# Performance work log

Hardware: AMD Instinct MI355X
Metric: run time of the kernel (lower is better)

Reference implementation:

```python
import jax, jax.numpy as jnp
import numpy as np

B, C, C2, E = 4, 1024, 1024, 1024
D = 1024          # context_size (d_q = d_kv)
NH = 16           # module's n_heads arg -> actual head_dim after the quirky view
G = D // NH       # effective number of head groups = 64


def setup_inputs() -> dict:
    key = jax.random.key(0)
    ks = jax.random.split(key, 6)
    s = 0.02
    return {
        "x1": jax.random.normal(ks[0], (B, C, E), dtype=jnp.float32),
        "x2": jax.random.normal(ks[1], (B, C2, E), dtype=jnp.float32),
        "W_q": jax.random.normal(ks[2], (E, D), dtype=jnp.float32) * s,
        "W_k": jax.random.normal(ks[3], (E, D), dtype=jnp.float32) * s,
        "W_v": jax.random.normal(ks[4], (E, D), dtype=jnp.float32) * s,
        "W_o": jax.random.normal(ks[5], (D, D), dtype=jnp.float32) * s,
    }


def _split_heads(t):
    # (B, S, D) -> view (B, S, G, NH) -> transpose(1,2) -> (B, G, S, NH)
    b, s, _ = t.shape
    return jnp.transpose(t.reshape(b, s, G, NH), (0, 2, 1, 3))


def reference(x1, x2, W_q, W_k, W_v, W_o):
    Q = _split_heads(x1 @ W_q)   # (B, G, C, NH)
    K = _split_heads(x2 @ W_k)   # (B, G, C2, NH)
    V = _split_heads(x2 @ W_v)   # (B, G, C2, NH)
    scale = 1.0 / jnp.sqrt(jnp.asarray(NH, dtype=Q.dtype))
    scores = jnp.einsum("bgqh,bgkh->bgqk", Q, K) * scale  # (B, G, C, C2)
    w = jax.nn.softmax(scores, axis=-1)
    out = jnp.einsum("bgqk,bgkh->bgqh", w, V)             # (B, G, C, NH)
    out = jnp.transpose(out, (0, 2, 1, 3)).reshape(B, C, D)
    return out @ W_o  # dropout p=0 -> identity
```

## Files before the change

kernel.cpp:

```cpp
#include <hip/hip_runtime.h>


typedef _Float16 f16x8 __attribute__((ext_vector_type(8)));
typedef _Float16 f16x4 __attribute__((ext_vector_type(4)));
typedef _Float16 f16x2 __attribute__((ext_vector_type(2)));
typedef float    f32x4 __attribute__((ext_vector_type(4)));
typedef float    f32x16 __attribute__((ext_vector_type(16)));

#define GLOAD_LDS16(gp, lp)                                              \
    __builtin_amdgcn_global_load_lds(                                    \
        (const __attribute__((address_space(1))) void*)(gp),             \
        (__attribute__((address_space(3))) void*)(lp), 16, 0, 0)

static __device__ __forceinline__ f16x8 pack8f(const float* p) {
    f16x2 a = __builtin_bit_cast(f16x2, __builtin_amdgcn_cvt_pkrtz(p[0], p[1]));
    f16x2 b = __builtin_bit_cast(f16x2, __builtin_amdgcn_cvt_pkrtz(p[2], p[3]));
    f16x2 c = __builtin_bit_cast(f16x2, __builtin_amdgcn_cvt_pkrtz(p[4], p[5]));
    f16x2 d = __builtin_bit_cast(f16x2, __builtin_amdgcn_cvt_pkrtz(p[6], p[7]));
    f16x8 r;
    r[0] = a[0]; r[1] = a[1]; r[2] = b[0]; r[3] = b[1];
    r[4] = c[0]; r[5] = c[1]; r[6] = d[0]; r[7] = d[1];
    return r;
}

__global__ __launch_bounds__(256) void prep_kernel(
        const float* __restrict__ x1, const float* __restrict__ x2,
        const float* __restrict__ W0, const float* __restrict__ W1,
        const float* __restrict__ W2, const float* __restrict__ W3,
        _Float16* __restrict__ y1, _Float16* __restrict__ y2,
        _Float16* __restrict__ T0, _Float16* __restrict__ T1,
        _Float16* __restrict__ T2, _Float16* __restrict__ T3) {
    int bx = blockIdx.x, tid = threadIdx.x;
    if (bx < 8192) {
        int i = bx * 256 + tid;
        const float* x = (i < 1048576) ? x1 : x2;
        _Float16* y = (i < 1048576) ? y1 : y2;
        int j = i & 1048575;
        float4 v = ((const float4*)x)[j];
        f16x4 h = { (_Float16)v.x, (_Float16)v.y, (_Float16)v.z, (_Float16)v.w };
        ((f16x4*)y)[j] = h;
    } else {
        int z = (bx - 8192) >> 10;
        const float* W = (z == 0) ? W0 : (z == 1) ? W1 : (z == 2) ? W2 : W3;
        _Float16* WT = (z == 0) ? T0 : (z == 1) ? T1 : (z == 2) ? T2 : T3;
        int t = (bx - 8192) & 1023;
        int c0 = (t & 31) * 32, r0 = (t >> 5) * 32;
        __shared__ float tile[32][33];
        int tx = tid & 31, ty = tid >> 5;
#pragma unroll
        for (int i = 0; i < 32; i += 8)
            tile[ty + i][tx] = W[(r0 + ty + i) * 1024 + (c0 + tx)];
        __syncthreads();
#pragma unroll
        for (int i = 0; i < 32; i += 8)
            WT[(c0 + ty + i) * 1024 + (r0 + tx)] = (_Float16)tile[tx][ty + i];
    }
}

template <int MT, bool OUTF32>
static __device__ __forceinline__ void gemm_body(const _Float16* __restrict__ Atile,
                                                 const _Float16* __restrict__ BTtile,
                                                 void* __restrict__ Ctile,
                                                 _Float16* As, _Float16* Bs) {
    constexpr int AF = MT / 32;
    const int tid = threadIdx.x, lane = tid & 63, wave = tid >> 6;
    const int wm = wave >> 1, wn = wave & 1;
    const int col = lane & 15, quad = lane >> 4;

    f32x4 acc[AF][4];
#pragma unroll
    for (int i = 0; i < AF; i++)
#pragma unroll
        for (int j = 0; j < 4; j++) acc[i][j] = (f32x4){0.f, 0.f, 0.f, 0.f};

    const int srow = wave * 8 + (lane >> 3);
    const int sch = (lane & 7) * 8;
    const _Float16* Ag = Atile + (size_t)srow * 1024 + sch;
    const _Float16* Bg = BTtile + (size_t)srow * 1024 + sch;
    _Float16* Asl = As + wave * 512;
    _Float16* Bsl = Bs + wave * 512;

    for (int kt = 0; kt < 16; kt++) {
        __syncthreads();
#pragma unroll
        for (int c = 0; c < AF; c++)
            GLOAD_LDS16(Ag + (size_t)(c * 32) * 1024 + kt * 64, Asl + c * 2048);
#pragma unroll
        for (int c = 0; c < 4; c++)
            GLOAD_LDS16(Bg + (size_t)(c * 32) * 1024 + kt * 64, Bsl + c * 2048);
        __syncthreads();
#pragma unroll
        for (int ki = 0; ki < 2; ki++) {
            f16x8 af[AF], bf[4];
#pragma unroll
            for (int i = 0; i < AF; i++)
                af[i] = *(const f16x8*)(As + (wm * (MT / 2) + i * 16 + col) * 64 + ki * 32 + quad * 8);
#pragma unroll
            for (int j = 0; j < 4; j++)
                bf[j] = *(const f16x8*)(Bs + (wn * 64 + j * 16 + col) * 64 + ki * 32 + quad * 8);
#pragma unroll
            for (int i = 0; i < AF; i++)
#pragma unroll
                for (int j = 0; j < 4; j++)
                    acc[i][j] = __builtin_amdgcn_mfma_f32_16x16x32_f16(af[i], bf[j], acc[i][j], 0, 0, 0);
        }
    }

#pragma unroll
    for (int i = 0; i < AF; i++)
#pragma unroll
        for (int ii = 0; ii < 4; ii++) {
            int row = wm * (MT / 2) + i * 16 + quad * 4 + ii;
#pragma unroll
            for (int j = 0; j < 4; j++) {
                int cc = wn * 64 + j * 16 + col;
                if (OUTF32) ((float*)Ctile)[(size_t)row * 1024 + cc] = acc[i][j][ii];
                else ((_Float16*)Ctile)[(size_t)row * 1024 + cc] = (_Float16)acc[i][j][ii];
            }
        }
}

__global__ __launch_bounds__(256, 3) void gemm_qkv_kernel(
        const _Float16* __restrict__ x1h, const _Float16* __restrict__ x2h,
        const _Float16* __restrict__ WqT, const _Float16* __restrict__ WkvT,
        _Float16* __restrict__ Qh, _Float16* __restrict__ Kh, _Float16* __restrict__ Vh) {
    __shared__ _Float16 As[128 * 64], Bs[128 * 64];
    int gx = blockIdx.x;
    const _Float16 *A, *BT;
    _Float16* C;
    int m0, n0;
    if (gx < 256) {
        m0 = (gx >> 3) * 128; n0 = (gx & 7) * 128;
        A = x1h; BT = WqT + (size_t)n0 * 1024; C = Qh + n0;
    } else {
        int idx = gx - 256;
        m0 = (idx >> 4) * 128;
        int nb = idx & 15;
        n0 = nb * 128;
        A = x2h; BT = WkvT + (size_t)n0 * 1024;
        C = (nb < 8) ? (Kh + n0) : (Vh + (n0 - 1024));
    }
    gemm_body<128, false>(A + (size_t)m0 * 1024, BT, (void*)(C + (size_t)m0 * 1024), As, Bs);
}

__global__ __launch_bounds__(256, 4) void gemm_wo_kernel(const _Float16* __restrict__ Ah,
                                                         const _Float16* __restrict__ WoT,
                                                         float* __restrict__ out) {
    __shared__ _Float16 As[64 * 64], Bs[128 * 64];
    int gx = blockIdx.x;
    int m0 = (gx >> 3) * 64, n0 = (gx & 7) * 128;
    gemm_body<64, true>(Ah + (size_t)m0 * 1024, WoT + (size_t)n0 * 1024,
                        (void*)(out + (size_t)m0 * 1024 + n0), As, Bs);
}

__global__ __launch_bounds__(256, 8) void attn_kernel(const _Float16* __restrict__ Qh,
                                                      const _Float16* __restrict__ Kh,
                                                      const _Float16* __restrict__ Vh,
                                                      _Float16* __restrict__ Ah) {
    int pair = blockIdx.y;
    int b = pair >> 6, g = pair & 63;
    __shared__ _Float16 KA[2048];
    __shared__ _Float16 VA[2048];
    __shared__ _Float16 ones[8];

    const _Float16* Kg = Kh + (size_t)(b * 1024) * 1024 + g * 16;
    const _Float16* Vg = Vh + (size_t)(b * 1024) * 1024 + g * 16;
    int tid = threadIdx.x;
    if (tid < 8) ones[tid] = (_Float16)1.f;

    int lane = tid & 63, wave = tid >> 6;
    int n = lane & 31, h5 = lane >> 5;
    int q0 = blockIdx.x * 128 + wave * 32;

    f16x8 qf;
    {
        f16x8 t = *(const f16x8*)(Qh + (size_t)(b * 1024 + q0 + n) * 1024 + g * 16 + h5 * 8);
#pragma unroll
        for (int j = 0; j < 8; j++) qf[j] = (_Float16)((float)t[j] * 0.360673760f);
    }

    f32x16 acc = {0.f, 0.f, 0.f, 0.f, 0.f, 0.f, 0.f, 0.f,
                  0.f, 0.f, 0.f, 0.f, 0.f, 0.f, 0.f, 0.f};
    const f32x16 zero16 = acc;
    const _Float16* vbase = (n < 16) ? (VA + (n + 16 * h5) * 8) : ones;
    const int vstep = (n < 16) ? 256 : 0;

    const int krow = tid >> 1, kpart = tid & 1;
    const int kpm = (krow & 19) | ((krow & 4) << 1) | ((krow & 8) >> 1);
    const int kdst = (((krow >> 5) * 64) + kpm + 32 * kpart) * 8;
    const int vk0 = (tid >> 1) * 2 & 127, vpart = tid & 1;
    const int vbase_w = (vk0 >> 4) * 256 + ((vk0 >> 3) & 1) * 128 + vpart * 64 + (vk0 & 7);

    for (int c = 0; c < 8; c++) {
        if (c) __syncthreads();
        *(uint4*)(KA + kdst) =
            *(const uint4*)(Kg + (size_t)(c * 128 + krow) * 1024 + kpart * 8);
        if (tid < 128) {
            f16x8 v0 = *(const f16x8*)(Vg + (size_t)(c * 128 + vk0) * 1024 + vpart * 8);
            f16x8 v1 = *(const f16x8*)(Vg + (size_t)(c * 128 + vk0 + 1) * 1024 + vpart * 8);
#pragma unroll
            for (int j = 0; j < 8; j++) {
                f16x2 pr; pr[0] = v0[j]; pr[1] = v1[j];
                *(f16x2*)(VA + vbase_w + j * 8) = pr;
            }
        }
        __syncthreads();

#pragma unroll
        for (int t = 0; t < 4; t++) {
            f16x8 ak = *(const f16x8*)(KA + (t * 64 + lane) * 8);
            f32x16 s = __builtin_amdgcn_mfma_f32_32x32x16_f16(ak, qf, zero16, 0, 0, 0);
            float p[16];
#pragma unroll
            for (int i = 0; i < 16; i++) p[i] = __builtin_amdgcn_exp2f(s[i]);
            f16x8 pb0 = pack8f(p);
            f16x8 pb1 = pack8f(p + 8);
            f16x8 av0 = *(const f16x8*)(vbase + (2 * t) * vstep);
            f16x8 av1 = *(const f16x8*)(vbase + (2 * t + 1) * vstep);
            acc = __builtin_amdgcn_mfma_f32_32x32x16_f16(av0, pb0, acc, 0, 0, 0);
            acc = __builtin_amdgcn_mfma_f32_32x32x16_f16(av1, pb1, acc, 0, 0, 0);
        }
    }

    float rl = 1.0f / acc[8];
    f16x4 o0, o1;
#pragma unroll
    for (int i = 0; i < 4; i++) o0[i] = (_Float16)(acc[i] * rl);
#pragma unroll
    for (int i = 0; i < 4; i++) o1[i] = (_Float16)(acc[4 + i] * rl);
    _Float16* ob = Ah + (size_t)(b * 1024 + q0 + n) * 1024 + g * 16 + h5 * 4;
    *(f16x4*)(ob) = o0;
    *(f16x4*)(ob + 8) = o1;
}

extern "C" void kernel_launch(void* const* d_in, const int* in_sizes, int n_in,
                              void* d_out, int out_size, void* d_ws, size_t ws_size,
                              hipStream_t stream) {
    const float* x1 = (const float*)d_in[0];
    const float* x2 = (const float*)d_in[1];
    const float* Wq = (const float*)d_in[2];
    const float* Wk = (const float*)d_in[3];
    const float* Wv = (const float*)d_in[4];
    const float* Wo = (const float*)d_in[5];

    char* ws = (char*)d_ws;
    const size_t MB = 1u << 20;
    if (ws_size < 56 * MB) return;

    _Float16* x1h = (_Float16*)(ws + 0 * MB);
    _Float16* x2h = (_Float16*)(ws + 8 * MB);
    _Float16* WqT = (_Float16*)(ws + 16 * MB);
    _Float16* WkT = (_Float16*)(ws + 18 * MB);
    _Float16* WvT = (_Float16*)(ws + 20 * MB);
    _Float16* WoT = (_Float16*)(ws + 22 * MB);
    _Float16* Qh  = (_Float16*)(ws + 24 * MB);
    _Float16* Kh  = (_Float16*)(ws + 32 * MB);
    _Float16* Vh  = (_Float16*)(ws + 40 * MB);
    _Float16* Ah  = (_Float16*)(ws + 48 * MB);

    prep_kernel<<<12288, 256, 0, stream>>>(x1, x2, Wq, Wk, Wv, Wo,
                                           x1h, x2h, WqT, WkT, WvT, WoT);

    gemm_qkv_kernel<<<768, 256, 0, stream>>>(x1h, x2h, WqT, WkT, Qh, Kh, Vh);

    attn_kernel<<<dim3(8, 256), 256, 0, stream>>>(Qh, Kh, Vh, Ah);

    gemm_wo_kernel<<<512, 256, 0, stream>>>(Ah, WoT, (float*)d_out);
}
```

Before: 196.0 us.

## Prefetch next K/V chunk into registers, swizzle V LDS layout, reorder attention grid

The attention kernel now loads the next 128-key K/V chunk into registers while the current chunk is being computed, so global memory latency overlaps with MFMA and exp work. The V tile in LDS gets an XOR swizzle on both the write and read paths to reduce bank conflicts. Wave priority is raised around the compute section, and the grid axes are swapped so consecutive blocks cover different (batch, group) pairs rather than different query tiles. This costs extra registers for the prefetch buffers and precomputed offsets, which may lower occupancy.

```diff
diff --git a/kernel.cpp b/kernel.cpp
--- a/kernel.cpp
+++ b/kernel.cpp
@@ -157,7 +157,7 @@
                                                       const _Float16* __restrict__ Kh,
                                                       const _Float16* __restrict__ Vh,
                                                       _Float16* __restrict__ Ah) {
-    int pair = blockIdx.y;
+    int pair = blockIdx.x;
     int b = pair >> 6, g = pair & 63;
     __shared__ _Float16 KA[2048];
     __shared__ _Float16 VA[2048];
@@ -170,7 +170,7 @@
 
     int lane = tid & 63, wave = tid >> 6;
     int n = lane & 31, h5 = lane >> 5;
-    int q0 = blockIdx.x * 128 + wave * 32;
+    int q0 = blockIdx.y * 128 + wave * 32;
 
     f16x8 qf;
     {
@@ -182,30 +182,49 @@
     f32x16 acc = {0.f, 0.f, 0.f, 0.f, 0.f, 0.f, 0.f, 0.f,
                   0.f, 0.f, 0.f, 0.f, 0.f, 0.f, 0.f, 0.f};
     const f32x16 zero16 = acc;
-    const _Float16* vbase = (n < 16) ? (VA + (n + 16 * h5) * 8) : ones;
-    const int vstep = (n < 16) ? 256 : 0;
 
     const int krow = tid >> 1, kpart = tid & 1;
     const int kpm = (krow & 19) | ((krow & 4) << 1) | ((krow & 8) >> 1);
     const int kdst = (((krow >> 5) * 64) + kpm + 32 * kpart) * 8;
     const int vk0 = (tid >> 1) * 2 & 127, vpart = tid & 1;
-    const int vbase_w = (vk0 >> 4) * 256 + ((vk0 >> 3) & 1) * 128 + vpart * 64 + (vk0 & 7);
+    const int vbw2 = (((vk0 >> 4) * 256 + ((vk0 >> 3) & 1) * 128 + vpart * 64 + (vk0 & 7)))
+                   ^ (((vk0 >> 3) & 7) << 3);
+
+    int vaoff[8];
+#pragma unroll
+    for (int s = 0; s < 8; s++) {
+        int nsw = (n & 8) | ((n & 7) ^ (((s & 3) << 1) | h5));
+        vaoff[s] = (n < 16) ? ((s >> 2) * 1024 + (s & 3) * 256 + h5 * 128 + nsw * 8) : 0;
+    }
+    const _Float16* vrb = (n < 16) ? VA : ones;
+
+    uint4 kreg;
+    f16x8 v0, v1;
+    kreg = *(const uint4*)(Kg + (size_t)krow * 1024 + kpart * 8);
+    if (tid < 128) {
+        v0 = *(const f16x8*)(Vg + (size_t)vk0 * 1024 + vpart * 8);
+        v1 = *(const f16x8*)(Vg + (size_t)(vk0 + 1) * 1024 + vpart * 8);
+    }
 
     for (int c = 0; c < 8; c++) {
-        if (c) __syncthreads();
-        *(uint4*)(KA + kdst) =
-            *(const uint4*)(Kg + (size_t)(c * 128 + krow) * 1024 + kpart * 8);
+        __syncthreads();
+        *(uint4*)(KA + kdst) = kreg;
         if (tid < 128) {
-            f16x8 v0 = *(const f16x8*)(Vg + (size_t)(c * 128 + vk0) * 1024 + vpart * 8);
-            f16x8 v1 = *(const f16x8*)(Vg + (size_t)(c * 128 + vk0 + 1) * 1024 + vpart * 8);
 #pragma unroll
             for (int j = 0; j < 8; j++) {
                 f16x2 pr; pr[0] = v0[j]; pr[1] = v1[j];
-                *(f16x2*)(VA + vbase_w + j * 8) = pr;
+                *(f16x2*)(VA + (vbw2 ^ (j * 8))) = pr;
             }
         }
         __syncthreads();
-
+        if (c < 7) {
+            kreg = *(const uint4*)(Kg + (size_t)((c + 1) * 128 + krow) * 1024 + kpart * 8);
+            if (tid < 128) {
+                v0 = *(const f16x8*)(Vg + (size_t)((c + 1) * 128 + vk0) * 1024 + vpart * 8);
+                v1 = *(const f16x8*)(Vg + (size_t)((c + 1) * 128 + vk0 + 1) * 1024 + vpart * 8);
+            }
+        }
+        __builtin_amdgcn_s_setprio(1);
 #pragma unroll
         for (int t = 0; t < 4; t++) {
             f16x8 ak = *(const f16x8*)(KA + (t * 64 + lane) * 8);
@@ -215,11 +234,12 @@
             for (int i = 0; i < 16; i++) p[i] = __builtin_amdgcn_exp2f(s[i]);
             f16x8 pb0 = pack8f(p);
             f16x8 pb1 = pack8f(p + 8);
-            f16x8 av0 = *(const f16x8*)(vbase + (2 * t) * vstep);
-            f16x8 av1 = *(const f16x8*)(vbase + (2 * t + 1) * vstep);
+            f16x8 av0 = *(const f16x8*)(vrb + vaoff[2 * t]);
+            f16x8 av1 = *(const f16x8*)(vrb + vaoff[2 * t + 1]);
             acc = __builtin_amdgcn_mfma_f32_32x32x16_f16(av0, pb0, acc, 0, 0, 0);
             acc = __builtin_amdgcn_mfma_f32_32x32x16_f16(av1, pb1, acc, 0, 0, 0);
         }
+        __builtin_amdgcn_s_setprio(0);
     }
 
     float rl = 1.0f / acc[8];
@@ -263,7 +283,7 @@
 
     gemm_qkv_kernel<<<768, 256, 0, stream>>>(x1h, x2h, WqT, WkT, Qh, Kh, Vh);
 
-    attn_kernel<<<dim3(8, 256), 256, 0, stream>>>(Qh, Kh, Vh, Ah);
+    attn_kernel<<<dim3(256, 8), 256, 0, stream>>>(Qh, Kh, Vh, Ah);
 
     gemm_wo_kernel<<<512, 256, 0, stream>>>(Ah, WoT, (float*)d_out);
 }
```

New measurement: 212.6 us. +8.5%, slower.
